# Kernel optimization log

Measured on AMD Instinct MI355X. Metric: run time of the kernel, lower is better.

Reference implementation:

```python
import jax, jax.numpy as jnp
import numpy as np

N_NODES = 50000
BETA = 0.5
NEG_SLOPE = 0.2


def gat_conv(x, src, dst, W, a_src, a_dst, b):
    """Single-head GAT-style conv: gather, attend, softmax-per-dst, scatter-sum."""
    h = x @ W                                   # [N, F]
    as_ = h @ a_src                             # [N]
    ad_ = h @ a_dst                             # [N]
    e = jax.nn.leaky_relu(as_[src] + ad_[dst], NEG_SLOPE)  # [E]
    # numerically stable softmax over incoming edges of each dst node
    m = jax.ops.segment_max(e, dst, num_segments=N_NODES)  # [N]
    ex = jnp.exp(e - m[dst])                    # [E]
    denom = jax.ops.segment_sum(ex, dst, num_segments=N_NODES)  # [N]
    w = ex / denom[dst]                         # [E]
    out = jax.ops.segment_sum(w[:, None] * h[src], dst, num_segments=N_NODES)
    return out + b


def setup_inputs() -> dict:
    key = jax.random.key(0)
    ks = jax.random.split(key, 8)
    F_in, F_out = 64, 64
    x = jax.random.normal(ks[0], (N_NODES, F_in), dtype=jnp.float32)
    edge_index = jax.random.randint(ks[1], (2, 1600000), 0, N_NODES, dtype=jnp.int64)
    W = jax.random.normal(ks[2], (F_in, F_in), dtype=jnp.float32) * (1.0 / np.sqrt(F_in))
    a_src = jax.random.normal(ks[3], (F_in,), dtype=jnp.float32) * (1.0 / np.sqrt(F_in))
    a_dst = jax.random.normal(ks[4], (F_in,), dtype=jnp.float32) * (1.0 / np.sqrt(F_in))
    b = jnp.zeros((F_in,), dtype=jnp.float32)
    fc_w = jax.random.normal(ks[5], (F_in, F_out), dtype=jnp.float32) * (1.0 / np.sqrt(F_in))
    fc_b = jnp.zeros((F_out,), dtype=jnp.float32)
    return {"x": x, "edge_index": edge_index, "W": W, "a_src": a_src,
            "a_dst": a_dst, "b": b, "fc_w": fc_w, "fc_b": fc_b}


def reference(x, edge_index, W, a_src, a_dst, b, fc_w, fc_b):
    src, dst = edge_index[0], edge_index[1]
    x1 = BETA * gat_conv(x, src, dst, W, a_src, a_dst, b) + (1.0 - BETA) * x
    x2 = BETA * gat_conv(x1, src, dst, W, a_src, a_dst, b) + (1.0 - BETA) * x
    x3 = BETA * gat_conv(x2, src, dst, W, a_src, a_dst, b) + (1.0 - BETA) * x
    h = x3
    out = x3 @ fc_w + fc_b
    return (out, h)
```

## Files before the change

kernel.cpp:

```cpp
#include <hip/hip_runtime.h>
#include <hip/hip_bf16.h>
#include <math.h>

#define N_NODES 50000
#define FDIM 64
#define BETA 0.5f
#define NEG_SLOPE 0.2f

typedef __attribute__((ext_vector_type(8))) short bf16x8;
typedef __attribute__((ext_vector_type(4))) float f32x4;

__device__ __forceinline__ unsigned short f2bf(float f) {
    unsigned u = __float_as_uint(f);
    unsigned r = (u + 0x7FFFu + ((u >> 16) & 1u)) >> 16;
    return (unsigned short)r;
}
__device__ __forceinline__ float bf2f(unsigned short s) {
    return __uint_as_float((unsigned)s << 16);
}

#define CHUNK 4096
__global__ __launch_bounds__(256) void scatter_pairs(
    const unsigned int* __restrict__ eiu, int* __restrict__ gCursor,
    unsigned int* __restrict__ pairs, int E, int CAP) {
    __shared__ int det;
    __shared__ unsigned int staged[CHUNK];
    __shared__ unsigned short tmpd[CHUNK];
    __shared__ int hist[256], sc[256], lbase[256], gbase[256], lcur[256];
    int t = threadIdx.x;
    if (t == 0) det = 0;
    hist[t] = 0;
    __syncthreads();
    int beg = blockIdx.x * CHUNK;
    int end = min(E, beg + CHUNK);
    int n = end - beg;
    {
        int idx = beg + t;
        if (idx < E && eiu[2 * idx + 1] != 0u) atomicOr(&det, 1);
    }
    __syncthreads();
    bool is32 = det != 0;
    for (int i = beg + t; i < end; i += 256) {
        int d = is32 ? (int)eiu[E + i] : (int)eiu[2 * (size_t)(E + i)];
        tmpd[i - beg] = (unsigned short)d;
        atomicAdd(&hist[d >> 8], 1);
    }
    __syncthreads();
    sc[t] = hist[t];
    __syncthreads();
    for (int off = 1; off < 256; off <<= 1) {
        int v = (t >= off) ? sc[t - off] : 0;
        __syncthreads();
        sc[t] += v;
        __syncthreads();
    }
    int excl = sc[t] - hist[t];
    lbase[t] = excl;
    lcur[t] = excl;
    if (hist[t] > 0) gbase[t] = t * CAP + atomicAdd(&gCursor[t], hist[t]);
    __syncthreads();
    for (int i = beg + t; i < end; i += 256) {
        unsigned s = is32 ? eiu[i] : eiu[2 * (size_t)i];
        unsigned td = tmpd[i - beg];
        int b = (int)(td >> 8);
        int lp = atomicAdd(&lcur[b], 1);
        staged[lp] = s | (td << 16);
    }
    __syncthreads();
    for (int j = t; j < n; j += 256) {
        unsigned w = staged[j];
        int b = (int)(w >> 24);
        pairs[gbase[b] + (j - lbase[b])] = w;
    }
}

__global__ __launch_bounds__(1024) void bucket_sort(
    const unsigned int* __restrict__ pairs, const int* __restrict__ gCursor,
    int* __restrict__ offsets, unsigned short* __restrict__ srcs,
    int* __restrict__ degCnt, int N, int E, int CAP) {
    __shared__ int scb[256], cnt[256], sc[256], lcur[256], dh[256];
    __shared__ unsigned short sorted16[16384];
    int b = blockIdx.x, t = threadIdx.x;
    if (t < 256) { scb[t] = gCursor[t]; dh[t] = 0; }
    __syncthreads();
    for (int off = 1; off < 256; off <<= 1) {
        int v = (t < 256 && t >= off) ? scb[t - off] : 0;
        __syncthreads();
        if (t < 256) scb[t] += v;
        __syncthreads();
    }
    int cntb = gCursor[b];
    int beg = scb[b] - cntb;
    int pbase = b * CAP;
    bool useLds = cntb <= 16384;
    if (b == 0 && t == 0) offsets[N] = E;
    if (t < 256) cnt[t] = 0;
    __syncthreads();
    for (int i = t; i < cntb; i += 1024) atomicAdd(&cnt[(pairs[pbase + i] >> 16) & 255u], 1);
    __syncthreads();
    if (t < 256) {
        sc[t] = cnt[t];
        int node = (b << 8) + t;
        if (node < N) atomicAdd(&dh[min(cnt[t], 255)], 1);
    }
    __syncthreads();
    if (t < 256 && dh[t]) atomicAdd(&degCnt[t], dh[t]);
    for (int off = 1; off < 256; off <<= 1) {
        int v = (t < 256 && t >= off) ? sc[t - off] : 0;
        __syncthreads();
        if (t < 256) sc[t] += v;
        __syncthreads();
    }
    if (t < 256) {
        int excl = sc[t] - cnt[t];
        int node = (b << 8) + t;
        if (node < N) offsets[node] = beg + excl;
        lcur[t] = excl;
    }
    __syncthreads();
    if (useLds) {
        for (int i = t; i < cntb; i += 1024) {
            unsigned p = pairs[pbase + i];
            int lp = atomicAdd(&lcur[(p >> 16) & 255u], 1);
            sorted16[lp] = (unsigned short)(p & 0xFFFFu);
        }
        __syncthreads();
        for (int j = t; j < cntb; j += 1024) srcs[beg + j] = sorted16[j];
    } else {
        for (int i = t; i < cntb; i += 1024) {
            unsigned p = pairs[pbase + i];
            int lp = atomicAdd(&lcur[(p >> 16) & 255u], 1);
            srcs[beg + lp] = (unsigned short)(p & 0xFFFFu);
        }
    }
}

__global__ __launch_bounds__(256) void deg_scan(int* degCnt) {
    __shared__ int sc[256];
    int t = threadIdx.x;
    int c = degCnt[t];
    sc[t] = c;
    __syncthreads();
    for (int off = 1; off < 256; off <<= 1) {
        int v = (t >= off) ? sc[t - off] : 0;
        __syncthreads();
        sc[t] += v;
        __syncthreads();
    }
    degCnt[t] = sc[t] - c;
}

#define DCHUNK 2048
__global__ __launch_bounds__(256) void deg_scatter(
    const int* __restrict__ offsets, int* __restrict__ degCnt,
    int* __restrict__ perm, int N) {
    __shared__ int lh[256], lbase[256], lcur[256];
    int t = threadIdx.x;
    int beg = blockIdx.x * DCHUNK;
    int end = min(N, beg + DCHUNK);
    lh[t] = 0;
    lcur[t] = 0;
    __syncthreads();
    for (int i = beg + t; i < end; i += 256) {
        int d = min(offsets[i + 1] - offsets[i], 255);
        atomicAdd(&lh[d], 1);
    }
    __syncthreads();
    if (lh[t] > 0) lbase[t] = atomicAdd(&degCnt[t], lh[t]);
    __syncthreads();
    for (int i = beg + t; i < end; i += 256) {
        int d = min(offsets[i + 1] - offsets[i], 255);
        int r = atomicAdd(&lcur[d], 1);
        perm[lbase[d] + r] = i;
    }
}

__global__ __launch_bounds__(256) void prep_weights(
    const float* __restrict__ W, const float* __restrict__ fcw,
    unsigned short* __restrict__ WTh, unsigned short* __restrict__ WTl,
    unsigned short* __restrict__ FTh, unsigned short* __restrict__ FTl) {
    for (int idx = blockIdx.x * 256 + threadIdx.x; idx < 4096; idx += gridDim.x * 256) {
        int k = idx >> 6, f = idx & 63;
        float w = W[idx];
        unsigned short hi = f2bf(w);
        WTh[f * 64 + k] = hi;
        WTl[f * 64 + k] = f2bf(w - bf2f(hi));
        float w2 = fcw[idx];
        unsigned short hi2 = f2bf(w2);
        FTh[f * 64 + k] = hi2;
        FTl[f * 64 + k] = f2bf(w2 - bf2f(hi2));
    }
}

__global__ __launch_bounds__(256, 4) void transform_mfma(
    const float* __restrict__ x,
    const unsigned short* __restrict__ WTh, const unsigned short* __restrict__ WTl,
    const float* __restrict__ a_src, const float* __restrict__ a_dst,
    const float* __restrict__ bias,
    unsigned short* __restrict__ hb,
    float* __restrict__ fout,
    float* __restrict__ as_, float* __restrict__ ad_, int N) {
    __shared__ __align__(16) unsigned short WThs[64 * 72];
    __shared__ __align__(16) unsigned short WTls[64 * 72];
    int tid = threadIdx.x;
    {
        int row = tid >> 2;
        int ch = (tid & 3) * 16;
        uint4 h0 = ((const uint4*)(WTh + row * 64 + ch))[0];
        uint4 h1 = ((const uint4*)(WTh + row * 64 + ch))[1];
        uint4 l0 = ((const uint4*)(WTl + row * 64 + ch))[0];
        uint4 l1 = ((const uint4*)(WTl + row * 64 + ch))[1];
        *((uint4*)(WThs + row * 72 + ch)) = h0;
        *((uint4*)(WThs + row * 72 + ch + 8)) = h1;
        *((uint4*)(WTls + row * 72 + ch)) = l0;
        *((uint4*)(WTls + row * 72 + ch + 8)) = l1;
    }

    int wid = tid >> 6;
    int lane = tid & 63;
    int col = lane & 15;
    int quad = lane >> 4;
    int mbase = blockIdx.x * 64 + wid * 16;

    bf16x8 Ah[2], Al[2];
    int arow = mbase + col;
    const float* xr = x + (size_t)(arow < N ? arow : 0) * FDIM + quad * 8;
#pragma unroll
    for (int ks = 0; ks < 2; ks++) {
        float4 xa = *(const float4*)(xr + ks * 32);
        float4 xb = *(const float4*)(xr + ks * 32 + 4);
        float xv[8] = {xa.x, xa.y, xa.z, xa.w, xb.x, xb.y, xb.z, xb.w};
#pragma unroll
        for (int e = 0; e < 8; e++) {
            unsigned short hi = f2bf(xv[e]);
            Ah[ks][e] = (short)hi;
            Al[ks][e] = (short)f2bf(xv[e] - bf2f(hi));
        }
    }
    __syncthreads();

    f32x4 acc[4];
#pragma unroll
    for (int ft = 0; ft < 4; ft++) acc[ft] = (f32x4){0.f, 0.f, 0.f, 0.f};

#pragma unroll
    for (int ft = 0; ft < 4; ft++) {
        int f = ft * 16 + col;
#pragma unroll
        for (int ks = 0; ks < 2; ks++) {
            int off = f * 72 + ks * 32 + quad * 8;
            bf16x8 Bh = *(const bf16x8*)(WThs + off);
            bf16x8 Bl = *(const bf16x8*)(WTls + off);
            acc[ft] = __builtin_amdgcn_mfma_f32_16x16x32_bf16(Ah[ks], Bh, acc[ft], 0, 0, 0);
            acc[ft] = __builtin_amdgcn_mfma_f32_16x16x32_bf16(Ah[ks], Bl, acc[ft], 0, 0, 0);
            acc[ft] = __builtin_amdgcn_mfma_f32_16x16x32_bf16(Al[ks], Bh, acc[ft], 0, 0, 0);
        }
    }

    if (fout) {
#pragma unroll
        for (int ft = 0; ft < 4; ft++) {
            int f = ft * 16 + col;
            float bv = bias ? bias[f] : 0.f;
#pragma unroll
            for (int r = 0; r < 4; r++) {
                int node = mbase + quad * 4 + r;
                if (node < N) fout[(size_t)node * FDIM + f] = acc[ft][r] + bv;
            }
        }
    }
    if (hb) {
#pragma unroll
        for (int ft = 0; ft < 4; ft++) {
            int f = ft * 16 + col;
#pragma unroll
            for (int r = 0; r < 4; r++) {
                int node = mbase + quad * 4 + r;
                if (node < N) hb[(size_t)node * FDIM + f] = f2bf(acc[ft][r]);
            }
        }
    }
    if (as_) {
        float asv[4], adv[4];
#pragma unroll
        for (int ft = 0; ft < 4; ft++) {
            asv[ft] = a_src[ft * 16 + col];
            adv[ft] = a_dst[ft * 16 + col];
        }
#pragma unroll
        for (int r = 0; r < 4; r++) {
            float pa = 0.f, pd = 0.f;
#pragma unroll
            for (int ft = 0; ft < 4; ft++) {
                pa = fmaf(acc[ft][r], asv[ft], pa);
                pd = fmaf(acc[ft][r], adv[ft], pd);
            }
#pragma unroll
            for (int off = 1; off <= 8; off <<= 1) {
                pa += __shfl_xor(pa, off, 64);
                pd += __shfl_xor(pd, off, 64);
            }
            int node = mbase + quad * 4 + r;
            if (col == 0 && node < N) { as_[node] = pa; ad_[node] = pd; }
        }
    }
}

__device__ __forceinline__ void fma8(float* acc, float ex, const uint4& hv) {
    acc[0] = fmaf(ex, __uint_as_float(hv.x << 16), acc[0]);
    acc[1] = fmaf(ex, __uint_as_float(hv.x & 0xFFFF0000u), acc[1]);
    acc[2] = fmaf(ex, __uint_as_float(hv.y << 16), acc[2]);
    acc[3] = fmaf(ex, __uint_as_float(hv.y & 0xFFFF0000u), acc[3]);
    acc[4] = fmaf(ex, __uint_as_float(hv.z << 16), acc[4]);
    acc[5] = fmaf(ex, __uint_as_float(hv.z & 0xFFFF0000u), acc[5]);
    acc[6] = fmaf(ex, __uint_as_float(hv.w << 16), acc[6]);
    acc[7] = fmaf(ex, __uint_as_float(hv.w & 0xFFFF0000u), acc[7]);
}

__global__ __launch_bounds__(256) void gat_gather(
    const unsigned short* __restrict__ hb,
    const float* __restrict__ as_, const float* __restrict__ ad_,
    const int* __restrict__ offsets, const unsigned short* __restrict__ srcs,
    const int* __restrict__ perm,
    const float* __restrict__ bvec, const float* __restrict__ x0,
    float* __restrict__ xout, int N) {
    int wid = (blockIdx.x * blockDim.x + threadIdx.x) >> 6;
    int lane = threadIdx.x & 63;
    int g = lane >> 3;
    int q = lane & 7;
    int ni = wid * 8 + g;
    bool active = ni < N;
    int node = active ? perm[ni] : 0;
    int beg = active ? offsets[node] : 0;
    int end = active ? offsets[node + 1] : 0;
    float adv = active ? ad_[node] : 0.f;
    int mx = end - beg;
    mx = max(mx, __shfl_xor(mx, 8, 64));
    mx = max(mx, __shfl_xor(mx, 16, 64));
    mx = max(mx, __shfl_xor(mx, 32, 64));

    float acc[8];
#pragma unroll
    for (int k = 0; k < 8; k++) acc[k] = 0.f;
    float denom = 0.f;
    const unsigned short* hq = hb + (q << 3);

#define LRELU_EXP(E_) __expf((E_) > 0.f ? (E_) : NEG_SLOPE * (E_))

    for (int st = 0; st < mx; st += 8) {
        int i0 = beg + st;
        bool v[8];
        int s[8];
        uint4 hv[8];
        float ex[8];
#pragma unroll
        for (int k = 0; k < 8; k++) {
            v[k] = (i0 + k) < end;
            s[k] = (int)srcs[v[k] ? i0 + k : 0];
        }
#pragma unroll
        for (int k = 0; k < 8; k++) hv[k] = *(const uint4*)(hq + ((size_t)s[k] << 6));
#pragma unroll
        for (int k = 0; k < 8; k++) {
            float e = as_[s[k]] + adv;
            ex[k] = v[k] ? LRELU_EXP(e) : 0.f;
            denom += ex[k];
        }
#pragma unroll
        for (int k = 0; k < 8; k++) fma8(acc, ex[k], hv[k]);
    }
#undef LRELU_EXP

    if (active) {
        float inv = denom > 0.f ? 1.f / denom : 0.f;
        int fb = q * 8;
        f32x4 b0 = *(const f32x4*)(bvec + fb);
        f32x4 b1 = *(const f32x4*)(bvec + fb + 4);
        const float* x0r = x0 + (size_t)node * FDIM + fb;
        f32x4 x0a = *(const f32x4*)(x0r);
        f32x4 x0b = *(const f32x4*)(x0r + 4);
        f32x4 o0, o1;
        o0.x = BETA * (acc[0] * inv + b0.x) + (1.f - BETA) * x0a.x;
        o0.y = BETA * (acc[1] * inv + b0.y) + (1.f - BETA) * x0a.y;
        o0.z = BETA * (acc[2] * inv + b0.z) + (1.f - BETA) * x0a.z;
        o0.w = BETA * (acc[3] * inv + b0.w) + (1.f - BETA) * x0a.w;
        o1.x = BETA * (acc[4] * inv + b1.x) + (1.f - BETA) * x0b.x;
        o1.y = BETA * (acc[5] * inv + b1.y) + (1.f - BETA) * x0b.y;
        o1.z = BETA * (acc[6] * inv + b1.z) + (1.f - BETA) * x0b.z;
        o1.w = BETA * (acc[7] * inv + b1.w) + (1.f - BETA) * x0b.w;
        float* xr = xout + (size_t)node * FDIM + fb;
        *(f32x4*)(xr) = o0;
        *(f32x4*)(xr + 4) = o1;
    }
}

extern "C" void kernel_launch(void* const* d_in, const int* in_sizes, int n_in,
                              void* d_out, int out_size, void* d_ws, size_t ws_size,
                              hipStream_t stream) {
    const int N = N_NODES;
    const int E = in_sizes[1] / 2;
    const int NB = (N + 255) >> 8;
    const int CAP = (((E / N) * 256) * 2 + 1023) & ~1023;

    const float* x     = (const float*)d_in[0];
    const void*  ei    = d_in[1];
    const float* W     = (const float*)d_in[2];
    const float* a_src = (const float*)d_in[3];
    const float* a_dst = (const float*)d_in[4];
    const float* bvec  = (const float*)d_in[5];
    const float* fc_w  = (const float*)d_in[6];
    const float* fc_b  = (const float*)d_in[7];

    float* out = (float*)d_out;
    float* x3  = out + (size_t)N * FDIM;

    char* p = (char*)d_ws;
    auto alloc = [&](size_t bytes) -> void* {
        void* r = (void*)p;
        p += (bytes + 255) & ~(size_t)255;
        return r;
    };
    int*            gCursor  = (int*)alloc(512 * 4);
    unsigned int*   pairs    = (unsigned int*)alloc((size_t)256 * CAP * 4);
    unsigned short* srcs     = (unsigned short*)alloc((size_t)E * 2);
    int*            offsets  = (int*)alloc((size_t)(N + 1) * 4);
    int*            perm     = (int*)alloc((size_t)N * 4);
    float*          as_      = (float*)alloc((size_t)N * 4);
    float*          ad_      = (float*)alloc((size_t)N * 4);
    unsigned short* hbuf     = (unsigned short*)alloc((size_t)N * FDIM * 2);
    float*          xbuf     = (float*)alloc((size_t)N * FDIM * 4);
    unsigned short* WTh      = (unsigned short*)alloc(4096 * 2);
    unsigned short* WTl      = (unsigned short*)alloc(4096 * 2);
    unsigned short* FTh      = (unsigned short*)alloc(4096 * 2);
    unsigned short* FTl      = (unsigned short*)alloc(4096 * 2);
    int* degCnt = gCursor + 256;

    hipMemsetAsync(gCursor, 0, 512 * 4, stream);

    prep_weights<<<16, 256, 0, stream>>>(W, fc_w, WTh, WTl, FTh, FTl);

    scatter_pairs<<<(E + CHUNK - 1) / CHUNK, 256, 0, stream>>>(
        (const unsigned int*)ei, gCursor, pairs, E, CAP);
    bucket_sort<<<NB, 1024, 0, stream>>>(pairs, gCursor, offsets, srcs, degCnt, N, E, CAP);

    deg_scan<<<1, 256, 0, stream>>>(degCnt);
    deg_scatter<<<(N + DCHUNK - 1) / DCHUNK, 256, 0, stream>>>(offsets, degCnt, perm, N);

    int tgrid = (N + 63) / 64;
    int gwaves = (N + 7) / 8;
    int ggrid = (gwaves + 3) / 4;

    transform_mfma<<<tgrid, 256, 0, stream>>>(x, WTh, WTl, a_src, a_dst, nullptr,
                                              hbuf, nullptr, as_, ad_, N);
    gat_gather<<<ggrid, 256, 0, stream>>>(hbuf, as_, ad_, offsets, srcs, perm,
                                          bvec, x, xbuf, N);
    transform_mfma<<<tgrid, 256, 0, stream>>>(xbuf, WTh, WTl, a_src, a_dst, nullptr,
                                              hbuf, nullptr, as_, ad_, N);
    gat_gather<<<ggrid, 256, 0, stream>>>(hbuf, as_, ad_, offsets, srcs, perm,
                                          bvec, x, xbuf, N);
    transform_mfma<<<tgrid, 256, 0, stream>>>(xbuf, WTh, WTl, a_src, a_dst, nullptr,
                                              hbuf, nullptr, as_, ad_, N);
    gat_gather<<<ggrid, 256, 0, stream>>>(hbuf, as_, ad_, offsets, srcs, perm,
                                          bvec, x, x3, N);
    transform_mfma<<<tgrid, 256, 0, stream>>>(x3, FTh, FTl, nullptr, nullptr, fc_b,
                                              nullptr, out, nullptr, nullptr, N);
}
```

Measured before the change: 280.4 us.

## Sort per-node source lists and software-pipeline index loads in gather

```diff
diff --git a/kernel.cpp b/kernel.cpp
--- a/kernel.cpp
+++ b/kernel.cpp
@@ -133,6 +133,28 @@
             srcs[beg + lp] = (unsigned short)(p & 0xFFFFu);
         }
     }
+}
+
+__global__ __launch_bounds__(256) void src_sort(
+    const int* __restrict__ offsets, unsigned short* __restrict__ srcs, int N) {
+    int wv = (blockIdx.x * blockDim.x + threadIdx.x) >> 6;
+    if (wv >= N) return;
+    int lane = threadIdx.x & 63;
+    int beg = offsets[wv], end = offsets[wv + 1];
+    int deg = end - beg;
+    if (deg <= 1 || deg > 64) return;
+    unsigned v = (lane < deg) ? (unsigned)srcs[beg + lane] : 0xFFFFFFFFu;
+#pragma unroll
+    for (int k = 2; k <= 64; k <<= 1) {
+#pragma unroll
+        for (int j = k >> 1; j >= 1; j >>= 1) {
+            unsigned pv = __shfl_xor(v, j, 64);
+            bool up = ((lane & k) == 0);
+            bool takeMin = (((lane & j) == 0) == up);
+            v = takeMin ? min(v, pv) : max(v, pv);
+        }
+    }
+    if (lane < deg) srcs[beg + lane] = (unsigned short)v;
 }
 
 __global__ __launch_bounds__(256) void deg_scan(int* degCnt) {
@@ -333,8 +355,9 @@
     int node = active ? perm[ni] : 0;
     int beg = active ? offsets[node] : 0;
     int end = active ? offsets[node + 1] : 0;
+    int deg = end - beg;
     float adv = active ? ad_[node] : 0.f;
-    int mx = end - beg;
+    int mx = deg;
     mx = max(mx, __shfl_xor(mx, 8, 64));
     mx = max(mx, __shfl_xor(mx, 16, 64));
     mx = max(mx, __shfl_xor(mx, 32, 64));
@@ -347,27 +370,35 @@
 
 #define LRELU_EXP(E_) __expf((E_) > 0.f ? (E_) : NEG_SLOPE * (E_))
 
-    for (int st = 0; st < mx; st += 8) {
-        int i0 = beg + st;
-        bool v[8];
-        int s[8];
-        uint4 hv[8];
-        float ex[8];
-#pragma unroll
-        for (int k = 0; k < 8; k++) {
-            v[k] = (i0 + k) < end;
-            s[k] = (int)srcs[v[k] ? i0 + k : 0];
-        }
-#pragma unroll
-        for (int k = 0; k < 8; k++) hv[k] = *(const uint4*)(hq + ((size_t)s[k] << 6));
-#pragma unroll
-        for (int k = 0; k < 8; k++) {
-            float e = as_[s[k]] + adv;
-            ex[k] = v[k] ? LRELU_EXP(e) : 0.f;
-            denom += ex[k];
-        }
-#pragma unroll
-        for (int k = 0; k < 8; k++) fma8(acc, ex[k], hv[k]);
+    int p0 = (int)srcs[(0 < deg) ? beg + 0 : 0];
+    int p1 = (int)srcs[(1 < deg) ? beg + 1 : 0];
+    int p2 = (int)srcs[(2 < deg) ? beg + 2 : 0];
+    int p3 = (int)srcs[(3 < deg) ? beg + 3 : 0];
+
+    for (int st = 0; st < mx; st += 4) {
+        int ns = st + 4;
+        int n0 = (int)srcs[(ns + 0 < deg) ? beg + ns + 0 : 0];
+        int n1 = (int)srcs[(ns + 1 < deg) ? beg + ns + 1 : 0];
+        int n2 = (int)srcs[(ns + 2 < deg) ? beg + ns + 2 : 0];
+        int n3 = (int)srcs[(ns + 3 < deg) ? beg + ns + 3 : 0];
+        uint4 hv0 = *(const uint4*)(hq + ((size_t)p0 << 6));
+        uint4 hv1 = *(const uint4*)(hq + ((size_t)p1 << 6));
+        uint4 hv2 = *(const uint4*)(hq + ((size_t)p2 << 6));
+        uint4 hv3 = *(const uint4*)(hq + ((size_t)p3 << 6));
+        float e0 = as_[p0] + adv;
+        float e1 = as_[p1] + adv;
+        float e2 = as_[p2] + adv;
+        float e3 = as_[p3] + adv;
+        float ex0 = (st + 0 < deg) ? LRELU_EXP(e0) : 0.f;
+        float ex1 = (st + 1 < deg) ? LRELU_EXP(e1) : 0.f;
+        float ex2 = (st + 2 < deg) ? LRELU_EXP(e2) : 0.f;
+        float ex3 = (st + 3 < deg) ? LRELU_EXP(e3) : 0.f;
+        denom += (ex0 + ex1) + (ex2 + ex3);
+        fma8(acc, ex0, hv0);
+        fma8(acc, ex1, hv1);
+        fma8(acc, ex2, hv2);
+        fma8(acc, ex3, hv3);
+        p0 = n0; p1 = n1; p2 = n2; p3 = n3;
     }
 #undef LRELU_EXP
 
@@ -443,6 +474,7 @@
         (const unsigned int*)ei, gCursor, pairs, E, CAP);
     bucket_sort<<<NB, 1024, 0, stream>>>(pairs, gCursor, offsets, srcs, degCnt, N, E, CAP);
 
+    src_sort<<<(N + 3) / 4, 256, 0, stream>>>(offsets, srcs, N);
     deg_scan<<<1, 256, 0, stream>>>(degCnt);
     deg_scatter<<<(N + DCHUNK - 1) / DCHUNK, 256, 0, stream>>>(offsets, degCnt, perm, N);
 
```

New measurement: 265.5 us. 1.06x faster.
